# Optimization experiments

Measured on AMD Instinct MI355X. Metric: run time of the kernel, lower is better.

## Reference

```python
import jax, jax.numpy as jnp
import numpy as np

B, T, D, H, F = 4, 1024, 1024, 16, 4096
DH = D // H
EPS = 1e-5


def _ln(x, g, b):
    m = jnp.mean(x, axis=-1, keepdims=True)
    v = jnp.mean((x - m) ** 2, axis=-1, keepdims=True)
    return (x - m) * jax.lax.rsqrt(v + EPS) * g + b


def setup_inputs() -> dict:
    key = jax.random.key(0)
    ks = jax.random.split(key, 16)
    w = lambda k, s: jax.random.normal(k, s, jnp.float32) * 0.02
    return {
        "x": jax.random.normal(ks[0], (B, T, D), jnp.float32),
        "spatial_encoding": jax.random.normal(ks[1], (B, T, D), jnp.float32),
        "edge_encoding": jax.random.normal(ks[2], (B, T, D), jnp.float32),
        "ln1_g": jnp.ones((D,), jnp.float32), "ln1_b": jnp.zeros((D,), jnp.float32),
        "Wq": w(ks[3], (D, D)), "bq": jnp.zeros((D,), jnp.float32),
        "Wk": w(ks[4], (D, D)), "bk": jnp.zeros((D,), jnp.float32),
        "Wv": w(ks[5], (D, D)), "bv": jnp.zeros((D,), jnp.float32),
        "Wo": w(ks[6], (D, D)), "bo": jnp.zeros((D,), jnp.float32),
        "ln2_g": jnp.ones((D,), jnp.float32), "ln2_b": jnp.zeros((D,), jnp.float32),
        "W1": w(ks[7], (D, F)), "b1": jnp.zeros((F,), jnp.float32),
        "W2": w(ks[8], (F, D)), "b2": jnp.zeros((D,), jnp.float32),
        "lnb_g": jnp.ones((D,), jnp.float32), "lnb_b": jnp.zeros((D,), jnp.float32),
    }


def reference(x, spatial_encoding, edge_encoding, ln1_g, ln1_b,
              Wq, bq, Wk, bk, Wv, bv, Wo, bo, ln2_g, ln2_b,
              W1, b1, W2, b2, lnb_g, lnb_b):
    # pre-attention LayerNorm, residual taken post-norm (as in the torch code)
    x = _ln(x, ln1_g, ln1_b)
    residual = x
    # graph attention with spatial/edge score biases
    q = (x @ Wq + bq).reshape(B, T, H, DH)
    k = (x @ Wk + bk).reshape(B, T, H, DH)
    v = (x @ Wv + bv).reshape(B, T, H, DH)
    kb = k + spatial_encoding.reshape(B, T, H, DH) + edge_encoding.reshape(B, T, H, DH)
    scores = jnp.einsum('bthd,bshd->bhts', q, kb) / jnp.sqrt(jnp.float32(DH))
    attn = jax.nn.softmax(scores, axis=-1)  # (B, H, T, T)
    ctx = jnp.einsum('bhts,bshd->bthd', attn, v).reshape(B, T, D)
    x = ctx @ Wo + bo + residual
    x = _ln(x, ln2_g, ln2_b)
    # bottleneck FFN with residual + LayerNorm
    h = jax.nn.gelu(x @ W1 + b1) @ W2 + b2
    x = _ln(x + h, lnb_g, lnb_b)
    return (x, attn)
```

## Files before the change

### kernel.cpp

```cpp
#include <hip/hip_runtime.h>
#include <hip/hip_bf16.h>
#include <hip/hip_fp16.h>
#include <math.h>

#define B_ 4
#define T_ 1024
#define D_ 1024
#define H_ 16
#define DH_ 64
#define F_ 4096
#define BT_ (B_ * T_)
#define BTD ((size_t)B_ * T_ * D_)

typedef short bf16x8 __attribute__((ext_vector_type(8)));
typedef _Float16 f16x8 __attribute__((ext_vector_type(8)));
typedef float f32x4 __attribute__((ext_vector_type(4)));

__device__ __forceinline__ unsigned short f2b(float f) {
  __hip_bfloat16 h = __float2bfloat16(f);
  return *reinterpret_cast<unsigned short*>(&h);
}
__device__ __forceinline__ unsigned short f2h(float f) {
  __half h = __float2half(f);
  return *reinterpret_cast<unsigned short*>(&h);
}

__device__ __forceinline__ void gload16(const unsigned short* g, unsigned short* l) {
  __builtin_amdgcn_global_load_lds(
      (const __attribute__((address_space(1))) unsigned int*)(const void*)g,
      (__attribute__((address_space(3))) unsigned int*)(void*)l, 16, 0, 0);
}

__device__ __forceinline__ float gelu_f(float x) {
  float z2 = 1.5957691216057308f * (x + 0.044715f * x * x * x);
  return x / (1.0f + __expf(-z2));
}

__device__ __forceinline__ float blk_sum256(float v, float* s4) {
#pragma unroll
  for (int off = 32; off > 0; off >>= 1) v += __shfl_down(v, off);
  if ((threadIdx.x & 63) == 0) s4[threadIdx.x >> 6] = v;
  __syncthreads();
  float t = s4[0] + s4[1] + s4[2] + s4[3];
  __syncthreads();
  return t;
}

__global__ __launch_bounds__(256) void ln_rows(
    const float* __restrict__ in, const float* __restrict__ in2,
    const float* __restrict__ g, const float* __restrict__ bb,
    float* __restrict__ outf, unsigned short* __restrict__ outb) {
  __shared__ float s4[4];
  const size_t base = (size_t)blockIdx.x * D_;
  const int t = threadIdx.x;
  float4 v = ((const float4*)(in + base))[t];
  if (in2) {
    float4 w = ((const float4*)(in2 + base))[t];
    v.x += w.x; v.y += w.y; v.z += w.z; v.w += w.w;
  }
  float mean = blk_sum256(v.x + v.y + v.z + v.w, s4) * (1.0f / D_);
  float dx = v.x - mean, dy = v.y - mean, dz = v.z - mean, dw = v.w - mean;
  float var = blk_sum256(dx * dx + dy * dy + dz * dz + dw * dw, s4) * (1.0f / D_);
  float rstd = rsqrtf(var + 1e-5f);
  float4 gv = ((const float4*)g)[t];
  float4 bv = ((const float4*)bb)[t];
  float4 o;
  o.x = dx * rstd * gv.x + bv.x;
  o.y = dy * rstd * gv.y + bv.y;
  o.z = dz * rstd * gv.z + bv.z;
  o.w = dw * rstd * gv.w + bv.w;
  if (outf) ((float4*)(outf + base))[t] = o;
  if (outb) {
    unsigned short o4[4] = {f2b(o.x), f2b(o.y), f2b(o.z), f2b(o.w)};
    *(uint2*)(&outb[base + (size_t)t * 4]) = *(uint2*)o4;
  }
}

__global__ __launch_bounds__(256) void tcast_t(
    const float* __restrict__ in, unsigned short* __restrict__ out, int R, int C) {
  __shared__ unsigned short tile[32][33];
  const int c0 = blockIdx.x * 32, r0 = blockIdx.y * 32;
  const int col = threadIdx.x & 31, rq = threadIdx.x >> 5;
#pragma unroll
  for (int i = 0; i < 4; ++i) {
    int r = rq + i * 8;
    tile[r][col] = f2b(in[(size_t)(r0 + r) * C + c0 + col]);
  }
  __syncthreads();
#pragma unroll
  for (int i = 0; i < 4; ++i) {
    int r = rq + i * 8;
    out[(size_t)(c0 + r) * R + r0 + col] = tile[col][r];
  }
}

__global__ __launch_bounds__(256) void tcast4(
    const float* w0, const float* w1, const float* w2, const float* w3,
    unsigned short* o0, unsigned short* o1, unsigned short* o2, unsigned short* o3) {
  __shared__ unsigned short tile[32][33];
  const float* in = blockIdx.z == 0 ? w0 : blockIdx.z == 1 ? w1 : blockIdx.z == 2 ? w2 : w3;
  unsigned short* out = blockIdx.z == 0 ? o0 : blockIdx.z == 1 ? o1 : blockIdx.z == 2 ? o2 : o3;
  const int c0 = blockIdx.x * 32, r0 = blockIdx.y * 32;
  const int col = threadIdx.x & 31, rq = threadIdx.x >> 5;
#pragma unroll
  for (int i = 0; i < 4; ++i) {
    int r = rq + i * 8;
    tile[r][col] = f2b(in[(size_t)(r0 + r) * D_ + c0 + col]);
  }
  __syncthreads();
#pragma unroll
  for (int i = 0; i < 4; ++i) {
    int r = rq + i * 8;
    out[(size_t)(c0 + r) * D_ + r0 + col] = tile[col][r];
  }
}

__global__ __launch_bounds__(256, 4) void attn_fused(
    const unsigned short* __restrict__ qh, const unsigned short* __restrict__ kh,
    const unsigned short* __restrict__ vt, float* __restrict__ attn,
    unsigned short* __restrict__ ctxb) {
  __shared__ __align__(16) unsigned short Qs[64 * 64];
  __shared__ __align__(16) unsigned short Ks[64 * 64];
  __shared__ __align__(16) unsigned short Vs[64 * 64];
  __shared__ __align__(16) unsigned short Ps[64 * 64];
  const int tid = threadIdx.x;
  const int l = tid & 63, w = tid >> 6;
  const int wm = w >> 1, wn = w & 1;
  const int lk = l >> 4, lr = l & 15;
  const int bh = blockIdx.x, b = bh >> 4, h = bh & 15;
  const int tt = blockIdx.y;
  const unsigned short* Qg = qh + (size_t)b * T_ * D_ + h * DH_ + (size_t)tt * 64 * D_;
  const unsigned short* Kg = kh + (size_t)b * T_ * D_ + h * DH_;
  const unsigned short* Vg = vt + (size_t)bh * 64 * T_;

  const int ar = tid >> 3, ac = tid & 7;
  const int aswz = ((ac ^ (ar & 7)) << 3);

#pragma unroll
  for (int i = 0; i < 2; ++i)
    gload16(Qg + (size_t)(ar + 32 * i) * D_ + aswz, &Qs[(size_t)(i * 256 + tid) * 8]);
  __syncthreads();
  f16x8 qf[2][2];
#pragma unroll
  for (int mi = 0; mi < 2; ++mi) {
    const int row = wm * 32 + mi * 16 + lr;
#pragma unroll
    for (int kk = 0; kk < 2; ++kk)
      qf[mi][kk] = *(const f16x8*)&Qs[row * 64 + (((kk * 4 + lk) ^ (row & 7)) << 3)];
  }

  float lsum[2][4] = {};

  for (int st = 0; st < 16; ++st) {
    __syncthreads();
#pragma unroll
    for (int i = 0; i < 2; ++i)
      gload16(Kg + (size_t)(st * 64 + ar + 32 * i) * D_ + aswz, &Ks[(size_t)(i * 256 + tid) * 8]);
    __syncthreads();
    f16x8 kf[2][2];
#pragma unroll
    for (int ni = 0; ni < 2; ++ni) {
      const int row = wn * 32 + ni * 16 + lr;
#pragma unroll
      for (int kk = 0; kk < 2; ++kk)
        kf[ni][kk] = *(const f16x8*)&Ks[row * 64 + (((kk * 4 + lk) ^ (row & 7)) << 3)];
    }
    f32x4 acc[2][2] = {};
#pragma unroll
    for (int kk = 0; kk < 2; ++kk)
#pragma unroll
      for (int mi = 0; mi < 2; ++mi)
#pragma unroll
        for (int ni = 0; ni < 2; ++ni)
          acc[mi][ni] = __builtin_amdgcn_mfma_f32_16x16x32_f16(
              qf[mi][kk], kf[ni][kk], acc[mi][ni], 0, 0, 0);
#pragma unroll
    for (int mi = 0; mi < 2; ++mi)
#pragma unroll
      for (int r = 0; r < 4; ++r) {
        float v = __expf(acc[mi][0][r] * 0.125f) + __expf(acc[mi][1][r] * 0.125f);
        v += __shfl_xor(v, 1); v += __shfl_xor(v, 2);
        v += __shfl_xor(v, 4); v += __shfl_xor(v, 8);
        lsum[mi][r] += v;
      }
  }

  float* sL = (float*)Ps;
  if (lr == 0) {
#pragma unroll
    for (int mi = 0; mi < 2; ++mi)
#pragma unroll
      for (int r = 0; r < 4; ++r)
        sL[wn * 64 + wm * 32 + mi * 16 + lk * 4 + r] = lsum[mi][r];
  }
  __syncthreads();
  float rl[2][4];
#pragma unroll
  for (int mi = 0; mi < 2; ++mi)
#pragma unroll
    for (int r = 0; r < 4; ++r) {
      const int row = wm * 32 + mi * 16 + lk * 4 + r;
      rl[mi][r] = 1.0f / (sL[row] + sL[64 + row]);
    }
  __syncthreads();

  float* Cg = attn + (size_t)bh * T_ * T_;
  f32x4 cacc[2][2] = {};
  for (int st = 0; st < 16; ++st) {
    __syncthreads();
#pragma unroll
    for (int i = 0; i < 2; ++i) {
      gload16(Kg + (size_t)(st * 64 + ar + 32 * i) * D_ + aswz, &Ks[(size_t)(i * 256 + tid) * 8]);
      gload16(Vg + (size_t)(ar + 32 * i) * T_ + st * 64 + aswz, &Vs[(size_t)(i * 256 + tid) * 8]);
    }
    __syncthreads();
    f16x8 kf[2][2], vf[2][2];
#pragma unroll
    for (int ni = 0; ni < 2; ++ni) {
      const int row = wn * 32 + ni * 16 + lr;
#pragma unroll
      for (int kk = 0; kk < 2; ++kk) {
        kf[ni][kk] = *(const f16x8*)&Ks[row * 64 + (((kk * 4 + lk) ^ (row & 7)) << 3)];
        vf[ni][kk] = *(const f16x8*)&Vs[row * 64 + (((kk * 4 + lk) ^ (row & 7)) << 3)];
      }
    }
    f32x4 acc[2][2] = {};
#pragma unroll
    for (int kk = 0; kk < 2; ++kk)
#pragma unroll
      for (int mi = 0; mi < 2; ++mi)
#pragma unroll
        for (int ni = 0; ni < 2; ++ni)
          acc[mi][ni] = __builtin_amdgcn_mfma_f32_16x16x32_f16(
              qf[mi][kk], kf[ni][kk], acc[mi][ni], 0, 0, 0);
#pragma unroll
    for (int mi = 0; mi < 2; ++mi) {
      const int trow = wm * 32 + mi * 16 + lk * 4;
#pragma unroll
      for (int ni = 0; ni < 2; ++ni) {
        const int scol = wn * 32 + ni * 16 + lr;
#pragma unroll
        for (int r = 0; r < 4; ++r) {
          const int t = trow + r;
          float p = __expf(acc[mi][ni][r] * 0.125f) * rl[mi][r];
          __builtin_nontemporal_store(
              p, &Cg[(size_t)(tt * 64 + t) * T_ + (st * 64 + scol)]);
          Ps[t * 64 + (scol ^ ((t & 7) << 3))] = f2h(p);
        }
      }
    }
    __syncthreads();
#pragma unroll
    for (int kk = 0; kk < 2; ++kk) {
      f16x8 af[2];
#pragma unroll
      for (int mi = 0; mi < 2; ++mi) {
        const int row = wm * 32 + mi * 16 + lr;
        af[mi] = *(const f16x8*)&Ps[row * 64 + (((kk * 4 + lk) ^ (row & 7)) << 3)];
      }
#pragma unroll
      for (int mi = 0; mi < 2; ++mi)
#pragma unroll
        for (int ni = 0; ni < 2; ++ni)
          cacc[mi][ni] = __builtin_amdgcn_mfma_f32_16x16x32_f16(
              af[mi], vf[ni][kk], cacc[mi][ni], 0, 0, 0);
    }
  }

  unsigned short* Cb = ctxb + (size_t)b * T_ * D_ + h * DH_;
  const int crow0 = tt * 64 + wm * 32 + lk * 4;
  const int ccol0 = wn * 32 + lr;
#pragma unroll
  for (int mi = 0; mi < 2; ++mi)
#pragma unroll
    for (int ni = 0; ni < 2; ++ni)
#pragma unroll
      for (int r = 0; r < 4; ++r)
        Cb[(size_t)(crow0 + mi * 16 + r) * D_ + ccol0 + ni * 16] = f2b(cacc[mi][ni][r]);
}

template <int BN, int EPI, bool WF32, bool W16, bool FP16 = false, bool DB = false>
__global__ __launch_bounds__(256) void gemm_nt(
    const unsigned short* __restrict__ A, int lda,
    const unsigned short* __restrict__ Bm, int ldb,
    float* __restrict__ Cf, unsigned short* __restrict__ Cb, int ldc,
    const float* __restrict__ bias, const float* __restrict__ r1,
    const float* __restrict__ r2, float scale, int K) {
  constexpr int BM = 128, BK = 64;
  constexpr int WN = BN / 2;
  constexpr int FN = WN / 16;
  constexpr int NB = DB ? 4 : 1;
  static_assert(!DB || BN == 128, "counted vmcnt constants assume 8 loads/stage");
  __shared__ __align__(16) unsigned short As[NB][BM * BK];
  __shared__ __align__(16) unsigned short Bs[NB][BN * BK];
  const int tid = threadIdx.x;
  const int l = tid & 63;
  const int w = tid >> 6;
  const int wm = w >> 1, wn = w & 1;
  const int lr = l & 15, lk = l >> 4;
  const unsigned short* Ab = A + (size_t)blockIdx.y * BM * lda;
  const unsigned short* Bb = Bm + (size_t)blockIdx.x * BN * ldb;

  const int ar = tid >> 3;
  const int ac = tid & 7;
  const int aswz = ((ac ^ (ar & 7)) << 3);

  f32x4 acc[4][FN] = {};

  auto stage = [&](int buf, int k0) {
#pragma unroll
    for (int i = 0; i < 4; ++i)
      gload16(Ab + (size_t)(ar + 32 * i) * lda + k0 + aswz, &As[buf][(size_t)(i * 256 + tid) * 8]);
#pragma unroll
    for (int i = 0; i < BN / 32; ++i)
      gload16(Bb + (size_t)(ar + 32 * i) * ldb + k0 + aswz, &Bs[buf][(size_t)(i * 256 + tid) * 8]);
  };
  auto compute = [&](int buf) {
    bf16x8 af[4][2], bfr[FN][2];
#pragma unroll
    for (int mi = 0; mi < 4; ++mi) {
      const int row = wm * 64 + mi * 16 + lr;
#pragma unroll
      for (int kk = 0; kk < 2; ++kk)
        af[mi][kk] = *(const bf16x8*)&As[buf][row * BK + (((kk * 4 + lk) ^ (row & 7)) << 3)];
    }
#pragma unroll
    for (int ni = 0; ni < FN; ++ni) {
      const int row = wn * WN + ni * 16 + lr;
#pragma unroll
      for (int kk = 0; kk < 2; ++kk)
        bfr[ni][kk] = *(const bf16x8*)&Bs[buf][row * BK + (((kk * 4 + lk) ^ (row & 7)) << 3)];
    }
#pragma unroll
    for (int kk = 0; kk < 2; ++kk)
#pragma unroll
      for (int mi = 0; mi < 4; ++mi)
#pragma unroll
        for (int ni = 0; ni < FN; ++ni)
          acc[mi][ni] = __builtin_amdgcn_mfma_f32_16x16x32_bf16(
              af[mi][kk], bfr[ni][kk], acc[mi][ni], 0, 0, 0);
  };

  if constexpr (DB) {
    const int nt = K / BK;
    stage(0, 0);
    stage(1, BK);
    stage(2, 2 * BK);
    for (int t = 0; t < nt; ++t) {
      const int rem = nt - 1 - t;
      if (rem >= 2)      asm volatile("s_waitcnt vmcnt(16)" ::: "memory");
      else if (rem == 1) asm volatile("s_waitcnt vmcnt(8)" ::: "memory");
      else               asm volatile("s_waitcnt vmcnt(0)" ::: "memory");
      __builtin_amdgcn_s_barrier();
      __builtin_amdgcn_sched_barrier(0);
      if (t + 3 < nt) stage((t + 3) & 3, (t + 3) * BK);
      compute(t & 3);
    }
  } else {
    for (int k0 = 0; k0 < K; k0 += BK) {
      stage(0, k0);
      __syncthreads();
      compute(0);
      __syncthreads();
    }
  }

  const int crow0 = blockIdx.y * BM + wm * 64 + lk * 4;
  const int ccol0 = blockIdx.x * BN + wn * WN + lr;
  if constexpr (EPI == 5) {
#pragma unroll
    for (int mi = 0; mi < 4; ++mi)
#pragma unroll
      for (int ni = 0; ni < FN; ++ni) {
        const int row0 = crow0 + mi * 16;
        const int col = ccol0 + ni * 16;
        unsigned short __attribute__((aligned(8))) p4[4];
#pragma unroll
        for (int r = 0; r < 4; ++r) p4[r] = f2h(acc[mi][ni][r] + bias[col]);
        const int bidx = row0 >> 10, t0 = row0 & 1023;
        const int hh = col >> 6, j = col & 63;
        *(uint2*)&Cb[(((size_t)bidx * 16 + hh) * 64 + j) * T_ + t0] = *(uint2*)p4;
      }
  } else {
#pragma unroll
    for (int mi = 0; mi < 4; ++mi)
#pragma unroll
      for (int ni = 0; ni < FN; ++ni)
#pragma unroll
        for (int r = 0; r < 4; ++r) {
          const int row = crow0 + mi * 16 + r;
          const int col = ccol0 + ni * 16;
          float v = acc[mi][ni][r] * scale;
          if (EPI != 3) v += bias[col];
          if (EPI == 1) v = gelu_f(v);
          const size_t off = (size_t)row * ldc + col;
          if (EPI == 2) v += r1[off];
          if (EPI == 4) v += r1[off] + r2[off];
          if (WF32) Cf[off] = v;
          if (W16) Cb[off] = FP16 ? f2h(v) : f2b(v);
        }
  }
}

__global__ __launch_bounds__(256) void gemm_qkv(
    const unsigned short* __restrict__ A, const unsigned short* __restrict__ Wt,
    const float* __restrict__ bq, const float* __restrict__ bk,
    const float* __restrict__ bv, const float* __restrict__ sp,
    const float* __restrict__ ed, unsigned short* __restrict__ q_h,
    unsigned short* __restrict__ kb_h, unsigned short* __restrict__ vt) {
  constexpr int BM = 128, BN = 128, BK = 64, K = 1024;
  __shared__ __align__(16) unsigned short As[BM * BK];
  __shared__ __align__(16) unsigned short Bs[BN * BK];
  const int tid = threadIdx.x;
  const int l = tid & 63, w = tid >> 6;
  const int wm = w >> 1, wn = w & 1;
  const int lr = l & 15, lk = l >> 4;
  const unsigned short* Ab = A + (size_t)blockIdx.y * BM * D_;
  const unsigned short* Bb = Wt + (size_t)blockIdx.x * BN * D_;
  const int ar = tid >> 3, ac = tid & 7;
  const int aswz = ((ac ^ (ar & 7)) << 3);

  f32x4 acc[4][4] = {};
  for (int k0 = 0; k0 < K; k0 += BK) {
#pragma unroll
    for (int i = 0; i < 4; ++i) {
      gload16(Ab + (size_t)(ar + 32 * i) * D_ + k0 + aswz, &As[(size_t)(i * 256 + tid) * 8]);
      gload16(Bb + (size_t)(ar + 32 * i) * D_ + k0 + aswz, &Bs[(size_t)(i * 256 + tid) * 8]);
    }
    __syncthreads();
    bf16x8 af[4][2], bfr[4][2];
#pragma unroll
    for (int mi = 0; mi < 4; ++mi) {
      const int row = wm * 64 + mi * 16 + lr;
#pragma unroll
      for (int kk = 0; kk < 2; ++kk)
        af[mi][kk] = *(const bf16x8*)&As[row * BK + (((kk * 4 + lk) ^ (row & 7)) << 3)];
    }
#pragma unroll
    for (int ni = 0; ni < 4; ++ni) {
      const int row = wn * 64 + ni * 16 + lr;
#pragma unroll
      for (int kk = 0; kk < 2; ++kk)
        bfr[ni][kk] = *(const bf16x8*)&Bs[row * BK + (((kk * 4 + lk) ^ (row & 7)) << 3)];
    }
#pragma unroll
    for (int kk = 0; kk < 2; ++kk)
#pragma unroll
      for (int mi = 0; mi < 4; ++mi)
#pragma unroll
        for (int ni = 0; ni < 4; ++ni)
          acc[mi][ni] = __builtin_amdgcn_mfma_f32_16x16x32_bf16(
              af[mi][kk], bfr[ni][kk], acc[mi][ni], 0, 0, 0);
    __syncthreads();
  }

  const int seg = blockIdx.x >> 3;
  const float* bias = seg == 0 ? bq : seg == 1 ? bk : bv;
  const int crow0 = blockIdx.y * BM + wm * 64 + lk * 4;
  const int ccol0 = blockIdx.x * BN + wn * 64 + lr;
  if (seg == 2) {
#pragma unroll
    for (int mi = 0; mi < 4; ++mi)
#pragma unroll
      for (int ni = 0; ni < 4; ++ni) {
        const int row0 = crow0 + mi * 16;
        const int col = (ccol0 + ni * 16) & 1023;
        unsigned short __attribute__((aligned(8))) p4[4];
#pragma unroll
        for (int r = 0; r < 4; ++r) p4[r] = f2h(acc[mi][ni][r] + bias[col]);
        const int bidx = row0 >> 10, t0 = row0 & 1023;
        const int hh = col >> 6, j = col & 63;
        *(uint2*)&vt[(((size_t)bidx * 16 + hh) * 64 + j) * T_ + t0] = *(uint2*)p4;
      }
  } else {
    unsigned short* out = seg == 0 ? q_h : kb_h;
#pragma unroll
    for (int mi = 0; mi < 4; ++mi)
#pragma unroll
      for (int ni = 0; ni < 4; ++ni)
#pragma unroll
        for (int r = 0; r < 4; ++r) {
          const int row = crow0 + mi * 16 + r;
          const int col = (ccol0 + ni * 16) & 1023;
          float v = acc[mi][ni][r] + bias[col];
          const size_t off = (size_t)row * D_ + col;
          if (seg == 1) v += sp[off] + ed[off];
          out[off] = f2h(v);
        }
  }
}

extern "C" void kernel_launch(void* const* d_in, const int* in_sizes, int n_in,
                              void* d_out, int out_size, void* d_ws, size_t ws_size,
                              hipStream_t stream) {
  const float* x    = (const float*)d_in[0];
  const float* sp   = (const float*)d_in[1];
  const float* ed   = (const float*)d_in[2];
  const float* ln1g = (const float*)d_in[3];
  const float* ln1b = (const float*)d_in[4];
  const float* Wq   = (const float*)d_in[5];
  const float* bq   = (const float*)d_in[6];
  const float* Wk   = (const float*)d_in[7];
  const float* bk   = (const float*)d_in[8];
  const float* Wv   = (const float*)d_in[9];
  const float* bvv  = (const float*)d_in[10];
  const float* Wo   = (const float*)d_in[11];
  const float* bo   = (const float*)d_in[12];
  const float* ln2g = (const float*)d_in[13];
  const float* ln2b = (const float*)d_in[14];
  const float* W1   = (const float*)d_in[15];
  const float* b1   = (const float*)d_in[16];
  const float* W2   = (const float*)d_in[17];
  const float* b2   = (const float*)d_in[18];
  const float* lnbg = (const float*)d_in[19];
  const float* lnbb = (const float*)d_in[20];

  float* out_x = (float*)d_out;
  float* attn  = out_x + BTD;
  float* tt    = out_x;

  const size_t MB = 1 << 20;
  char* wsb = (char*)d_ws;
  float*          xn    = (float*)(wsb);
  unsigned short* xn_b  = (unsigned short*)(wsb + 16 * MB);
  unsigned short* WqT   = (unsigned short*)(wsb + 24 * MB);
  unsigned short* WkT   = (unsigned short*)(wsb + 26 * MB);
  unsigned short* WvT   = (unsigned short*)(wsb + 28 * MB);
  unsigned short* WoT   = (unsigned short*)(wsb + 30 * MB);
  unsigned short* W1T   = (unsigned short*)(wsb + 32 * MB);
  unsigned short* W2T   = (unsigned short*)(wsb + 40 * MB);
  unsigned short* q_h   = (unsigned short*)(wsb + 48 * MB);
  unsigned short* kb_h  = (unsigned short*)(wsb + 56 * MB);
  unsigned short* vt    = (unsigned short*)(wsb + 80 * MB);
  unsigned short* ctx_b = xn_b;
  unsigned short* h1_b  = (unsigned short*)(wsb + 48 * MB);
  float*          h2    = (float*)(wsb + 80 * MB);
  float*          y     = xn;
  unsigned short* y_b   = xn_b;

  dim3 blk(256);
  dim3 g_dd(8, 32);

  ln_rows<<<BT_, blk, 0, stream>>>(x, nullptr, ln1g, ln1b, xn, xn_b);
  tcast4<<<dim3(32, 32, 4), blk, 0, stream>>>(Wq, Wk, Wv, Wo, WqT, WkT, WvT, WoT);
  tcast_t<<<dim3(128, 32), blk, 0, stream>>>(W1, W1T, 1024, 4096);
  tcast_t<<<dim3(32, 128), blk, 0, stream>>>(W2, W2T, 4096, 1024);
  gemm_qkv<<<dim3(24, 32), blk, 0, stream>>>(
      xn_b, WqT, bq, bk, bvv, sp, ed, q_h, kb_h, vt);
  attn_fused<<<dim3(64, 16), blk, 0, stream>>>(q_h, kb_h, vt, attn, ctx_b);
  gemm_nt<128, 2, true, false, false, true><<<g_dd, blk, 0, stream>>>(
      ctx_b, D_, WoT, D_, tt, nullptr, D_, bo, xn, nullptr, 1.f, D_);
  ln_rows<<<BT_, blk, 0, stream>>>(tt, nullptr, ln2g, ln2b, y, y_b);
  gemm_nt<128, 1, false, true><<<dim3(32, 32), blk, 0, stream>>>(
      y_b, D_, W1T, D_, nullptr, h1_b, F_, b1, nullptr, nullptr, 1.f, D_);
  gemm_nt<128, 2, true, false, false, true><<<g_dd, blk, 0, stream>>>(
      h1_b, F_, W2T, F_, h2, nullptr, D_, b2, y, nullptr, 1.f, F_);
  ln_rows<<<BT_, blk, 0, stream>>>(h2, nullptr, lnbg, lnbb, out_x, nullptr);
}
```

Measured before the change: 367.1 us.

## Double-buffer K/V tiles in fused attention with explicit waitcnt pipelining

Shared memory in the fused attention kernel becomes five regions, so the next K tile (and V tile in the second pass) is prefetched into an alternate buffer while the current tile is computed. Full __syncthreads pairs are replaced by raw s_barrier with hand-counted vmcnt/lgkmcnt waits that also account for the outstanding attn-probability stores. The per-tile cross-lane shuffle reduction of row sums is moved out of the loop and done once at the end. This hides global-load latency and cuts barrier and shuffle overhead. The cost is more LDS per block and fragile hand-tuned wait counts.

```diff
diff --git a/kernel.cpp b/kernel.cpp
--- a/kernel.cpp
+++ b/kernel.cpp
@@ -119,10 +119,12 @@
     const unsigned short* __restrict__ qh, const unsigned short* __restrict__ kh,
     const unsigned short* __restrict__ vt, float* __restrict__ attn,
     unsigned short* __restrict__ ctxb) {
-  __shared__ __align__(16) unsigned short Qs[64 * 64];
-  __shared__ __align__(16) unsigned short Ks[64 * 64];
-  __shared__ __align__(16) unsigned short Vs[64 * 64];
-  __shared__ __align__(16) unsigned short Ps[64 * 64];
+  __shared__ __align__(16) unsigned short L[5 * 4096];
+  unsigned short* const R0 = L;
+  unsigned short* const R1 = L + 4096;
+  unsigned short* const R2 = L + 2 * 4096;
+  unsigned short* const R3 = L + 3 * 4096;
+  unsigned short* const R4 = L + 4 * 4096;
   const int tid = threadIdx.x;
   const int l = tid & 63, w = tid >> 6;
   const int wm = w >> 1, wn = w & 1;
@@ -136,34 +138,52 @@
   const int ar = tid >> 3, ac = tid & 7;
   const int aswz = ((ac ^ (ar & 7)) << 3);
 
+  auto stageK = [&](int st, unsigned short* buf) {
+#pragma unroll
+    for (int i = 0; i < 2; ++i)
+      gload16(Kg + (size_t)(st * 64 + ar + 32 * i) * D_ + aswz, &buf[(size_t)(i * 256 + tid) * 8]);
+  };
+  auto stageV = [&](int st, unsigned short* buf) {
+#pragma unroll
+    for (int i = 0; i < 2; ++i)
+      gload16(Vg + (size_t)(ar + 32 * i) * T_ + st * 64 + aswz, &buf[(size_t)(i * 256 + tid) * 8]);
+  };
+
 #pragma unroll
   for (int i = 0; i < 2; ++i)
-    gload16(Qg + (size_t)(ar + 32 * i) * D_ + aswz, &Qs[(size_t)(i * 256 + tid) * 8]);
-  __syncthreads();
+    gload16(Qg + (size_t)(ar + 32 * i) * D_ + aswz, &R0[(size_t)(i * 256 + tid) * 8]);
+  stageK(0, R1);
+  asm volatile("s_waitcnt vmcnt(2)" ::: "memory");
+  __builtin_amdgcn_s_barrier();
+  __builtin_amdgcn_sched_barrier(0);
   f16x8 qf[2][2];
 #pragma unroll
   for (int mi = 0; mi < 2; ++mi) {
     const int row = wm * 32 + mi * 16 + lr;
 #pragma unroll
     for (int kk = 0; kk < 2; ++kk)
-      qf[mi][kk] = *(const f16x8*)&Qs[row * 64 + (((kk * 4 + lk) ^ (row & 7)) << 3)];
+      qf[mi][kk] = *(const f16x8*)&R0[row * 64 + (((kk * 4 + lk) ^ (row & 7)) << 3)];
   }
 
   float lsum[2][4] = {};
 
   for (int st = 0; st < 16; ++st) {
-    __syncthreads();
-#pragma unroll
-    for (int i = 0; i < 2; ++i)
-      gload16(Kg + (size_t)(st * 64 + ar + 32 * i) * D_ + aswz, &Ks[(size_t)(i * 256 + tid) * 8]);
-    __syncthreads();
+    asm volatile("s_waitcnt lgkmcnt(0)" ::: "memory");
+    __builtin_amdgcn_s_barrier();
+    __builtin_amdgcn_sched_barrier(0);
+    if (st + 1 < 16) stageK(st + 1, ((st + 1) & 1) ? R2 : R1);
+    __builtin_amdgcn_sched_barrier(0);
+    if (st + 1 < 16) asm volatile("s_waitcnt vmcnt(2)" ::: "memory");
+    else             asm volatile("s_waitcnt vmcnt(0)" ::: "memory");
+    __builtin_amdgcn_sched_barrier(0);
+    const unsigned short* Kb = (st & 1) ? R2 : R1;
     f16x8 kf[2][2];
 #pragma unroll
     for (int ni = 0; ni < 2; ++ni) {
       const int row = wn * 32 + ni * 16 + lr;
 #pragma unroll
       for (int kk = 0; kk < 2; ++kk)
-        kf[ni][kk] = *(const f16x8*)&Ks[row * 64 + (((kk * 4 + lk) ^ (row & 7)) << 3)];
+        kf[ni][kk] = *(const f16x8*)&Kb[row * 64 + (((kk * 4 + lk) ^ (row & 7)) << 3)];
     }
     f32x4 acc[2][2] = {};
 #pragma unroll
@@ -177,15 +197,20 @@
 #pragma unroll
     for (int mi = 0; mi < 2; ++mi)
 #pragma unroll
-      for (int r = 0; r < 4; ++r) {
-        float v = __expf(acc[mi][0][r] * 0.125f) + __expf(acc[mi][1][r] * 0.125f);
-        v += __shfl_xor(v, 1); v += __shfl_xor(v, 2);
-        v += __shfl_xor(v, 4); v += __shfl_xor(v, 8);
-        lsum[mi][r] += v;
-      }
-  }
-
-  float* sL = (float*)Ps;
+      for (int r = 0; r < 4; ++r)
+        lsum[mi][r] += __expf(acc[mi][0][r] * 0.125f) + __expf(acc[mi][1][r] * 0.125f);
+  }
+#pragma unroll
+  for (int mi = 0; mi < 2; ++mi)
+#pragma unroll
+    for (int r = 0; r < 4; ++r) {
+      float v = lsum[mi][r];
+      v += __shfl_xor(v, 1); v += __shfl_xor(v, 2);
+      v += __shfl_xor(v, 4); v += __shfl_xor(v, 8);
+      lsum[mi][r] = v;
+    }
+
+  float* sL = (float*)R4;
   if (lr == 0) {
 #pragma unroll
     for (int mi = 0; mi < 2; ++mi)
@@ -193,7 +218,9 @@
       for (int r = 0; r < 4; ++r)
         sL[wn * 64 + wm * 32 + mi * 16 + lk * 4 + r] = lsum[mi][r];
   }
-  __syncthreads();
+  asm volatile("s_waitcnt lgkmcnt(0)" ::: "memory");
+  __builtin_amdgcn_s_barrier();
+  __builtin_amdgcn_sched_barrier(0);
   float rl[2][4];
 #pragma unroll
   for (int mi = 0; mi < 2; ++mi)
@@ -202,26 +229,37 @@
       const int row = wm * 32 + mi * 16 + lk * 4 + r;
       rl[mi][r] = 1.0f / (sL[row] + sL[64 + row]);
     }
-  __syncthreads();
+  asm volatile("s_waitcnt lgkmcnt(0)" ::: "memory");
+  __builtin_amdgcn_sched_barrier(0);
+  stageK(0, R1);
+  stageV(0, R2);
+  __builtin_amdgcn_sched_barrier(0);
 
   float* Cg = attn + (size_t)bh * T_ * T_;
   f32x4 cacc[2][2] = {};
   for (int st = 0; st < 16; ++st) {
-    __syncthreads();
-#pragma unroll
-    for (int i = 0; i < 2; ++i) {
-      gload16(Kg + (size_t)(st * 64 + ar + 32 * i) * D_ + aswz, &Ks[(size_t)(i * 256 + tid) * 8]);
-      gload16(Vg + (size_t)(ar + 32 * i) * T_ + st * 64 + aswz, &Vs[(size_t)(i * 256 + tid) * 8]);
-    }
-    __syncthreads();
+    asm volatile("s_waitcnt lgkmcnt(0)" ::: "memory");
+    __builtin_amdgcn_s_barrier();
+    __builtin_amdgcn_sched_barrier(0);
+    if (st + 1 < 16) {
+      stageK(st + 1, ((st + 1) & 1) ? R0 : R1);
+      stageV(st + 1, ((st + 1) & 1) ? R3 : R2);
+    }
+    __builtin_amdgcn_sched_barrier(0);
+    if (st == 0)      asm volatile("s_waitcnt vmcnt(4)" ::: "memory");
+    else if (st < 15) asm volatile("s_waitcnt vmcnt(20)" ::: "memory");
+    else              asm volatile("s_waitcnt vmcnt(16)" ::: "memory");
+    __builtin_amdgcn_sched_barrier(0);
+    const unsigned short* Kb = (st & 1) ? R0 : R1;
+    const unsigned short* Vb = (st & 1) ? R3 : R2;
     f16x8 kf[2][2], vf[2][2];
 #pragma unroll
     for (int ni = 0; ni < 2; ++ni) {
       const int row = wn * 32 + ni * 16 + lr;
 #pragma unroll
       for (int kk = 0; kk < 2; ++kk) {
-        kf[ni][kk] = *(const f16x8*)&Ks[row * 64 + (((kk * 4 + lk) ^ (row & 7)) << 3)];
-        vf[ni][kk] = *(const f16x8*)&Vs[row * 64 + (((kk * 4 + lk) ^ (row & 7)) << 3)];
+        kf[ni][kk] = *(const f16x8*)&Kb[row * 64 + (((kk * 4 + lk) ^ (row & 7)) << 3)];
+        vf[ni][kk] = *(const f16x8*)&Vb[row * 64 + (((kk * 4 + lk) ^ (row & 7)) << 3)];
       }
     }
     f32x4 acc[2][2] = {};
@@ -245,18 +283,20 @@
           float p = __expf(acc[mi][ni][r] * 0.125f) * rl[mi][r];
           __builtin_nontemporal_store(
               p, &Cg[(size_t)(tt * 64 + t) * T_ + (st * 64 + scol)]);
-          Ps[t * 64 + (scol ^ ((t & 7) << 3))] = f2h(p);
+          R4[t * 64 + (scol ^ ((t & 7) << 3))] = f2h(p);
         }
       }
     }
-    __syncthreads();
+    asm volatile("s_waitcnt lgkmcnt(0)" ::: "memory");
+    __builtin_amdgcn_s_barrier();
+    __builtin_amdgcn_sched_barrier(0);
 #pragma unroll
     for (int kk = 0; kk < 2; ++kk) {
       f16x8 af[2];
 #pragma unroll
       for (int mi = 0; mi < 2; ++mi) {
         const int row = wm * 32 + mi * 16 + lr;
-        af[mi] = *(const f16x8*)&Ps[row * 64 + (((kk * 4 + lk) ^ (row & 7)) << 3)];
+        af[mi] = *(const f16x8*)&R4[row * 64 + (((kk * 4 + lk) ^ (row & 7)) << 3)];
       }
 #pragma unroll
       for (int mi = 0; mi < 2; ++mi)
```

New measurement: 356.5 us. -2.9%, faster.
